# Performance work log

Measured on AMD Instinct MI355X. Metric: run time of the kernel, lower is better.

Reference implementation:

```python
import jax, jax.numpy as jnp
import numpy as np

HIDDEN = 1024
HEADS = 16
HEAD_DIM = HIDDEN // HEADS  # 64
BATCH = 2
SEQ = 2048
MASK_IDENTITY = True


def setup_inputs() -> dict:
    key = jax.random.key(0)
    ks = jax.random.split(key, 9)
    s = 1.0 / np.sqrt(HIDDEN)
    return {
        "hidden_states": jax.random.normal(ks[0], (BATCH, SEQ, HIDDEN), jnp.float32),
        "Wq": jax.random.normal(ks[1], (HIDDEN, HIDDEN), jnp.float32) * s,
        "bq": jnp.zeros((HIDDEN,), jnp.float32),
        "Wk": jax.random.normal(ks[2], (HIDDEN, HIDDEN), jnp.float32) * s,
        "bk": jnp.zeros((HIDDEN,), jnp.float32),
        "Wv": jax.random.normal(ks[3], (HIDDEN, HIDDEN), jnp.float32) * s,
        "bv": jnp.zeros((HIDDEN,), jnp.float32),
        "Wd": jax.random.normal(ks[4], (HIDDEN, HIDDEN), jnp.float32) * s,
        "bd": jnp.zeros((HIDDEN,), jnp.float32),
    }


def _split_heads(x):
    # [B, S, H*Dh] -> [B, H, S, Dh]
    b, s, _ = x.shape
    return x.reshape(b, s, HEADS, HEAD_DIM).transpose(0, 2, 1, 3)


def reference(hidden_states, Wq, bq, Wk, bk, Wv, bv, Wd, bd):
    # torch Linear: y = x @ W.T + b
    q = _split_heads(hidden_states @ Wq.T + bq)  # [B,H,S,Dh]
    k = _split_heads(hidden_states @ Wk.T + bk)
    v = _split_heads(hidden_states @ Wv.T + bv)

    scores = jnp.einsum("bhqd,bhkd->bhqk", q, k) / np.sqrt(HEAD_DIM)
    if MASK_IDENTITY:
        mask_value = -jnp.finfo(scores.dtype).max
        eye = jnp.eye(scores.shape[-1], dtype=bool)  # [S,S], broadcast over B,H
        scores = jnp.where(eye, mask_value, scores)
    probs = jax.nn.softmax(scores, axis=-1)
    ctx = jnp.einsum("bhqk,bhkd->bhqd", probs, v)  # [B,H,S,Dh]
    b, h, s, d = ctx.shape
    ctx = ctx.transpose(0, 2, 1, 3).reshape(b, s, h * d)  # [B,S,H*Dh]
    return ctx @ Wd.T + bd
```

## Files before the change

kernel.cpp:

```cpp
#include <hip/hip_runtime.h>
#include <hip/hip_bf16.h>
#include <stdint.h>

#define HIDDEN 1024
#define SEQL   2048
#define NB     2
#define NH     16
#define DH     64
#define MTOT   (NB * SEQL)
#define QKVLD  3072
#define SCALE_Q 0.18033688011112042f

typedef __bf16 bf16x8 __attribute__((ext_vector_type(8)));
typedef __bf16 bf16x4 __attribute__((ext_vector_type(4)));
typedef float  f32x4  __attribute__((ext_vector_type(4)));
typedef float  f32x16 __attribute__((ext_vector_type(16)));

__device__ __forceinline__ void gload16(const void* g, void* l) {
    __builtin_amdgcn_global_load_lds(
        (const __attribute__((address_space(1))) void*)g,
        (__attribute__((address_space(3))) void*)l, 16, 0, 0);
}
__device__ __forceinline__ float exp2fast(float x) {
    float r;
    asm("v_exp_f32 %0, %1" : "=v"(r) : "v"(x));
    return r;
}
__device__ __forceinline__ unsigned cvtpk(float lo, float hi) {
    unsigned r;
    asm("v_cvt_pk_bf16_f32 %0, %1, %2" : "=v"(r) : "v"(lo), "v"(hi));
    return r;
}
__device__ __forceinline__ void pswap(unsigned& a, unsigned& b) {
    asm volatile("v_permlane32_swap_b32 %0, %1" : "+v"(a), "+v"(b));
}

__global__ void prep(const float* __restrict__ H,
                     const float* __restrict__ Wq, const float* __restrict__ Wk,
                     const float* __restrict__ Wv, const float* __restrict__ Wd,
                     const float* __restrict__ bq, const float* __restrict__ bk,
                     const float* __restrict__ bv,
                     __bf16* __restrict__ Hb, __bf16* __restrict__ Wall,
                     float* __restrict__ bqkv) {
    const int bid = blockIdx.x, tid = threadIdx.x;
    if (bid < 4096) {
        int i = bid * 256 + tid;
        float4 v = reinterpret_cast<const float4*>(H)[i];
        bf16x4 o = { (__bf16)v.x, (__bf16)v.y, (__bf16)v.z, (__bf16)v.w };
        reinterpret_cast<bf16x4*>(Hb)[i] = o;
    } else if (bid < 8192) {
        int wi = bid - 4096;
        int seg = wi >> 10;
        int i = (wi & 1023) * 256 + tid;
        const float* src = seg == 0 ? Wq : seg == 1 ? Wk : seg == 2 ? Wv : Wd;
        float sc = (seg == 0) ? SCALE_Q : 1.0f;
        float4 v = reinterpret_cast<const float4*>(src)[i];
        bf16x4 o = { (__bf16)(v.x * sc), (__bf16)(v.y * sc),
                     (__bf16)(v.z * sc), (__bf16)(v.w * sc) };
        reinterpret_cast<bf16x4*>(Wall)[(size_t)seg * 262144 + i] = o;
    } else {
        for (int i = tid; i < 3072; i += 256) {
            float v = (i < 1024) ? bq[i] * SCALE_Q
                    : (i < 2048) ? bk[i - 1024] : bv[i - 2048];
            bqkv[i] = v;
        }
    }
}

__global__ __launch_bounds__(256) void transpose_v(const __bf16* __restrict__ QKV,
                                                   __bf16* __restrict__ Vt) {
    __shared__ __bf16 t[64][66];
    const int st = blockIdx.x, bh = blockIdx.y;
    const int b = bh >> 4, h = bh & 15;
    const int tid = threadIdx.x;
    const int r = tid >> 3, c = tid & 7;
    const __bf16* src = QKV + (size_t)(b * SEQL + st * 64) * QKVLD + 2048 + h * 64;
    *(int4*)&t[r][c * 8]      = *(const int4*)(src + (size_t)r * QKVLD + c * 8);
    *(int4*)&t[r + 32][c * 8] = *(const int4*)(src + (size_t)(r + 32) * QKVLD + c * 8);
    __syncthreads();
    __bf16* dst = Vt + (size_t)bh * DH * SEQL + st * 64;
    const int d = tid >> 3;
    __bf16 tmp0[8], tmp1[8];
#pragma unroll
    for (int j = 0; j < 8; ++j) {
        tmp0[j] = t[c * 8 + j][d];
        tmp1[j] = t[c * 8 + j][d + 32];
    }
    *(int4*)(dst + (size_t)d * SEQL + c * 8)        = *(int4*)tmp0;
    *(int4*)(dst + (size_t)(d + 32) * SEQL + c * 8) = *(int4*)tmp1;
}

__global__ __launch_bounds__(256) void gemm_qkv(const __bf16* __restrict__ A,
                                                const __bf16* __restrict__ Bw,
                                                const float* __restrict__ bias,
                                                __bf16* __restrict__ C) {
    __shared__ __bf16 As[128 * 32];
    __shared__ __bf16 Bs[128 * 32];
    const int K = 1024, N = QKVLD;

    int bid = blockIdx.x;
    int swz = (bid & 7) * 96 + (bid >> 3);
    const int bm = (swz & 31) * 128;
    const int bn = (swz >> 5) * 128;

    const int tid = threadIdx.x;
    const int w = tid >> 6, l = tid & 63, g = l >> 4, lc = l & 15;
    const int wr = (w >> 1) * 64, wc = (w & 1) * 64;
    const int row = tid >> 2, ch = tid & 3;

    const __bf16* Ap = A  + (size_t)(bm + row) * K + ch * 8;
    const __bf16* Bp = Bw + (size_t)(bn + row) * K + ch * 8;
    __bf16* AsLo = &As[w * 512];
    __bf16* AsHi = &As[2048 + w * 512];
    __bf16* BsLo = &Bs[w * 512];
    __bf16* BsHi = &Bs[2048 + w * 512];

    f32x4 acc[4][4];
    const f32x4 z4 = {0.f, 0.f, 0.f, 0.f};
#pragma unroll
    for (int i = 0; i < 4; ++i)
#pragma unroll
        for (int j = 0; j < 4; ++j) acc[i][j] = z4;

    for (int kt = 0; kt < K; kt += 32) {
        gload16(Ap + kt,                   AsLo);
        gload16(Ap + kt + (size_t)64 * K,  AsHi);
        gload16(Bp + kt,                   BsLo);
        gload16(Bp + kt + (size_t)64 * K,  BsHi);
        __syncthreads();

        bf16x8 af[4], bfr[4];
#pragma unroll
        for (int i = 0; i < 4; ++i)
            af[i] = *(const bf16x8*)&As[(wr + i * 16 + lc) * 32 + g * 8];
#pragma unroll
        for (int j = 0; j < 4; ++j)
            bfr[j] = *(const bf16x8*)&Bs[(wc + j * 16 + lc) * 32 + g * 8];
        __builtin_amdgcn_s_setprio(1);
#pragma unroll
        for (int i = 0; i < 4; ++i)
#pragma unroll
            for (int j = 0; j < 4; ++j)
                acc[i][j] = __builtin_amdgcn_mfma_f32_16x16x32_bf16(af[i], bfr[j], acc[i][j], 0, 0, 0);
        __builtin_amdgcn_s_setprio(0);
        __syncthreads();
    }

#pragma unroll
    for (int i = 0; i < 4; ++i) {
        int r0 = bm + wr + i * 16 + g * 4;
#pragma unroll
        for (int j = 0; j < 4; ++j) {
            int c = bn + wc + j * 16 + lc;
            float bb = bias[c];
#pragma unroll
            for (int r = 0; r < 4; ++r)
                C[(size_t)(r0 + r) * N + c] = (__bf16)(acc[i][j][r] + bb);
        }
    }
}

__global__ __launch_bounds__(256) void gemm_out(const __bf16* __restrict__ A,
                                                const __bf16* __restrict__ Bw,
                                                const float* __restrict__ bias,
                                                float* __restrict__ Cout) {
    __shared__ __bf16 As[64 * 32];
    __shared__ __bf16 Bs[128 * 32];
    const int K = 1024, N = 1024;

    int bid = blockIdx.x;
    int swz = (bid & 7) * 64 + (bid >> 3);
    const int bm = (swz & 63) * 64;
    const int bn = (swz >> 6) * 128;

    const int tid = threadIdx.x;
    const int w = tid >> 6, l = tid & 63, g = l >> 4, lc = l & 15;
    const int wr = (w >> 1) * 32, wc = (w & 1) * 64;
    const int row = tid >> 2, ch = tid & 3;

    const __bf16* Ap = A  + (size_t)(bm + row) * K + ch * 8;
    const __bf16* Bp = Bw + (size_t)(bn + row) * K + ch * 8;
    __bf16* AsW  = &As[w * 512];
    __bf16* BsLo = &Bs[w * 512];
    __bf16* BsHi = &Bs[2048 + w * 512];

    f32x4 acc[2][4];
    const f32x4 z4 = {0.f, 0.f, 0.f, 0.f};
#pragma unroll
    for (int i = 0; i < 2; ++i)
#pragma unroll
        for (int j = 0; j < 4; ++j) acc[i][j] = z4;

    for (int kt = 0; kt < K; kt += 32) {
        gload16(Ap + kt,                   AsW);
        gload16(Bp + kt,                   BsLo);
        gload16(Bp + kt + (size_t)64 * K,  BsHi);
        __syncthreads();

        bf16x8 af[2], bfr[4];
#pragma unroll
        for (int i = 0; i < 2; ++i)
            af[i] = *(const bf16x8*)&As[(wr + i * 16 + lc) * 32 + g * 8];
#pragma unroll
        for (int j = 0; j < 4; ++j)
            bfr[j] = *(const bf16x8*)&Bs[(wc + j * 16 + lc) * 32 + g * 8];
        __builtin_amdgcn_s_setprio(1);
#pragma unroll
        for (int i = 0; i < 2; ++i)
#pragma unroll
            for (int j = 0; j < 4; ++j)
                acc[i][j] = __builtin_amdgcn_mfma_f32_16x16x32_bf16(af[i], bfr[j], acc[i][j], 0, 0, 0);
        __builtin_amdgcn_s_setprio(0);
        __syncthreads();
    }

#pragma unroll
    for (int i = 0; i < 2; ++i) {
        int r0 = bm + wr + i * 16 + g * 4;
#pragma unroll
        for (int j = 0; j < 4; ++j) {
            int c = bn + wc + j * 16 + lc;
            float bb = bias[c];
#pragma unroll
            for (int r = 0; r < 4; ++r)
                Cout[(size_t)(r0 + r) * N + c] = acc[i][j][r] + bb;
        }
    }
}

__global__ __launch_bounds__(256) void attn_kernel(const __bf16* __restrict__ QKV,
                                                   const __bf16* __restrict__ Vt,
                                                   __bf16* __restrict__ Ctx) {
    __shared__ __bf16 k_lds[2][64][64];
    __shared__ __bf16 v_lds[2][64][64];
    __shared__ float  bc[4][32];

    const int tid = threadIdx.x;
    const int w  = tid >> 6;
    const int l  = tid & 63;
    const int ql = l & 31;
    const int lh = l >> 5;

    int bid = blockIdx.x;
    int swz = (bid & 7) * 64 + (bid >> 3);
    const int qt = swz & 15, bh = swz >> 4;
    const int b = bh >> 4, hd = bh & 15;
    const int qw = qt * 128 + w * 32;

    const __bf16* Qg = QKV + (size_t)b * SEQL * QKVLD + hd * DH;
    const __bf16* Kg = Qg + 1024;
    const __bf16* Vg = Vt + (size_t)bh * DH * SEQL;

    bf16x8 qf[4];
    {
        const __bf16* qp = Qg + (size_t)(qw + ql) * QKVLD + lh * 8;
#pragma unroll
        for (int c = 0; c < 4; ++c) qf[c] = *(const bf16x8*)(qp + c * 16);
    }

    const int sr   = l >> 3;
    const int gcol = ((l & 7) * 8) ^ (sr << 3);
    auto stage = [&](int kb, int nb) {
        const __bf16* kp = Kg + (size_t)(kb + w * 8 + sr) * QKVLD + gcol;
        const __bf16* vp = Vg + (size_t)(w * 8 + sr) * SEQL + kb + gcol;
        gload16(kp,                          &k_lds[nb][w * 8][0]);
        gload16(kp + (size_t)32 * QKVLD,     &k_lds[nb][32 + w * 8][0]);
        gload16(vp,                          &v_lds[nb][w * 8][0]);
        gload16(vp + (size_t)32 * SEQL,      &v_lds[nb][32 + w * 8][0]);
    };

    stage(0, 0);
    __syncthreads();

    f32x16 o0, o1;
#pragma unroll
    for (int r = 0; r < 16; ++r) { o0[r] = 0.f; o1[r] = 0.f; }
    float l8[8];
#pragma unroll
    for (int r = 0; r < 8; ++r) l8[r] = 0.f;

    f32x16 zc;
#pragma unroll
    for (int r = 0; r < 16; ++r) zc[r] = 0.f;

    const int NT = SEQL / 64;
    const int rsw = (ql & 7) << 3;

    for (int kt = 0; kt < NT; ++kt) {
        const int buf = kt & 1;
        const int kb = kt * 64;

        if (kt + 1 < NT) stage(kb + 64, buf ^ 1);

        f32x16 sA, sB;
        __builtin_amdgcn_s_setprio(1);
        {
            bf16x8 k0 = *(const bf16x8*)&k_lds[buf][ql]     [(lh * 8) ^ rsw];
            bf16x8 k1 = *(const bf16x8*)&k_lds[buf][32 + ql][(lh * 8) ^ rsw];
            sA = __builtin_amdgcn_mfma_f32_32x32x16_bf16(k0, qf[0], zc, 0, 0, 0);
            sB = __builtin_amdgcn_mfma_f32_32x32x16_bf16(k1, qf[0], zc, 0, 0, 0);
        }
#pragma unroll
        for (int c = 1; c < 4; ++c) {
            bf16x8 k0 = *(const bf16x8*)&k_lds[buf][ql]     [(c * 16 + lh * 8) ^ rsw];
            bf16x8 k1 = *(const bf16x8*)&k_lds[buf][32 + ql][(c * 16 + lh * 8) ^ rsw];
            sA = __builtin_amdgcn_mfma_f32_32x32x16_bf16(k0, qf[c], sA, 0, 0, 0);
            sB = __builtin_amdgcn_mfma_f32_32x32x16_bf16(k1, qf[c], sB, 0, 0, 0);
        }
        __builtin_amdgcn_s_setprio(0);

        if (kb < qw + 32 && qw < kb + 64) {
            const int qg = qw + ql;
#pragma unroll
            for (int i = 0; i < 16; ++i) {
                int kg = kb + (i & 3) + ((i >> 2) & 3) * 8 + lh * 4;
                if (kg == qg)      sA[i] = -1e30f;
                if (kg + 32 == qg) sB[i] = -1e30f;
            }
        }

#pragma unroll
        for (int i = 0; i < 16; ++i) sA[i] = exp2fast(sA[i]);
#pragma unroll
        for (int i = 0; i < 16; ++i) sB[i] = exp2fast(sB[i]);
#pragma unroll
        for (int i = 0; i < 8; ++i)
            l8[i] += (sA[i] + sA[i + 8]) + (sB[i] + sB[i + 8]);

        bf16x8 pa[4];
        {
            unsigned w0 = cvtpk(sA[0],  sA[1]);
            unsigned w1 = cvtpk(sA[2],  sA[3]);
            unsigned w2 = cvtpk(sA[4],  sA[5]);
            unsigned w3 = cvtpk(sA[6],  sA[7]);
            unsigned w4 = cvtpk(sA[8],  sA[9]);
            unsigned w5 = cvtpk(sA[10], sA[11]);
            unsigned w6 = cvtpk(sA[12], sA[13]);
            unsigned w7 = cvtpk(sA[14], sA[15]);
            pswap(w0, w2); pswap(w1, w3);
            pswap(w4, w6); pswap(w5, w7);
            uint4 lo4 = {w0, w1, w2, w3};
            uint4 hi4 = {w4, w5, w6, w7};
            pa[0] = *(bf16x8*)&lo4;
            pa[1] = *(bf16x8*)&hi4;
        }
        {
            unsigned w0 = cvtpk(sB[0],  sB[1]);
            unsigned w1 = cvtpk(sB[2],  sB[3]);
            unsigned w2 = cvtpk(sB[4],  sB[5]);
            unsigned w3 = cvtpk(sB[6],  sB[7]);
            unsigned w4 = cvtpk(sB[8],  sB[9]);
            unsigned w5 = cvtpk(sB[10], sB[11]);
            unsigned w6 = cvtpk(sB[12], sB[13]);
            unsigned w7 = cvtpk(sB[14], sB[15]);
            pswap(w0, w2); pswap(w1, w3);
            pswap(w4, w6); pswap(w5, w7);
            uint4 lo4 = {w0, w1, w2, w3};
            uint4 hi4 = {w4, w5, w6, w7};
            pa[2] = *(bf16x8*)&lo4;
            pa[3] = *(bf16x8*)&hi4;
        }

        __builtin_amdgcn_s_setprio(1);
#pragma unroll
        for (int s = 0; s < 2; ++s)
#pragma unroll
            for (int sl = 0; sl < 2; ++sl) {
                const int col = s * 32 + sl * 16 + lh * 8;
                bf16x8 v0 = *(const bf16x8*)&v_lds[buf][ql]     [col ^ rsw];
                bf16x8 v1 = *(const bf16x8*)&v_lds[buf][32 + ql][col ^ rsw];
                o0 = __builtin_amdgcn_mfma_f32_32x32x16_bf16(pa[s * 2 + sl], v0, o0, 0, 0, 0);
                o1 = __builtin_amdgcn_mfma_f32_32x32x16_bf16(pa[s * 2 + sl], v1, o1, 0, 0, 0);
            }
        __builtin_amdgcn_s_setprio(0);

        __syncthreads();
    }

    float l_r = ((l8[0] + l8[1]) + (l8[2] + l8[3]))
              + ((l8[4] + l8[5]) + (l8[6] + l8[7]));
    l_r += __shfl_xor(l_r, 32, 64);
    if (lh == 0) bc[w][ql] = 1.f / l_r;
    asm volatile("s_waitcnt lgkmcnt(0)" ::: "memory");
    __builtin_amdgcn_wave_barrier();
#pragma unroll
    for (int r = 0; r < 16; ++r) {
        int cr = (r & 3) + (r >> 2) * 8 + lh * 4;
        float iv = bc[w][cr];
        int qrow = qw + cr;
        __bf16* cp = Ctx + (size_t)(b * SEQL + qrow) * HIDDEN + hd * DH + ql;
        cp[0]  = (__bf16)(o0[r] * iv);
        cp[32] = (__bf16)(o1[r] * iv);
    }
}

extern "C" void kernel_launch(void* const* d_in, const int* in_sizes, int n_in,
                              void* d_out, int out_size, void* d_ws, size_t ws_size,
                              hipStream_t stream) {
    const float* H  = (const float*)d_in[0];
    const float* Wq = (const float*)d_in[1];
    const float* bq = (const float*)d_in[2];
    const float* Wk = (const float*)d_in[3];
    const float* bk = (const float*)d_in[4];
    const float* Wv = (const float*)d_in[5];
    const float* bv = (const float*)d_in[6];
    const float* Wd = (const float*)d_in[7];
    const float* bd = (const float*)d_in[8];
    float* out = (float*)d_out;

    char* ws = (char*)d_ws;
    const size_t MB = 1024 * 1024;
    __bf16* Hb    = (__bf16*)(ws + 0 * MB);
    __bf16* Ctx   = (__bf16*)(ws + 0 * MB);
    __bf16* Wqkvb = (__bf16*)(ws + 8 * MB);
    __bf16* Wdb   = (__bf16*)(ws + 14 * MB);
    float*  bqkv  = (float*) (ws + 16 * MB);
    __bf16* QKV   = (__bf16*)(ws + 17 * MB);
    __bf16* Vtb   = (__bf16*)(ws + 41 * MB);
    if (ws_size < 49 * MB) return;

    prep<<<8193, 256, 0, stream>>>(H, Wq, Wk, Wv, Wd, bq, bk, bv, Hb, Wqkvb, bqkv);

    gemm_qkv<<<768, 256, 0, stream>>>(Hb, Wqkvb, bqkv, QKV);

    transpose_v<<<dim3(32, 32), 256, 0, stream>>>(QKV, Vtb);

    attn_kernel<<<512, 256, 0, stream>>>(QKV, Vtb, Ctx);

    gemm_out<<<512, 256, 0, stream>>>(Ctx, Wdb, bd, out);
}
```

Before: 131.3 us.

## Double K-tile depth in QKV GEMM and attention key block size with swizzled LDS

The QKV projection GEMM now stages 64-wide K slices instead of 32, with an XOR-swizzled LDS layout, so it runs half as many barrier pairs per output tile. The attention kernel now stages 128 keys per iteration instead of 64 and processes them as two 64-key sub-blocks, with a new swizzle for the wider V tile. Both changes aim to cut synchronisation and loop overhead per unit of work. In exchange they double LDS use per block, which may lower occupancy.

```diff
diff --git a/kernel.cpp b/kernel.cpp
--- a/kernel.cpp
+++ b/kernel.cpp
@@ -94,8 +94,8 @@
                                                 const __bf16* __restrict__ Bw,
                                                 const float* __restrict__ bias,
                                                 __bf16* __restrict__ C) {
-    __shared__ __bf16 As[128 * 32];
-    __shared__ __bf16 Bs[128 * 32];
+    __shared__ __bf16 As[128 * 64];
+    __shared__ __bf16 Bs[128 * 64];
     const int K = 1024, N = QKVLD;
 
     int bid = blockIdx.x;
@@ -106,14 +106,13 @@
     const int tid = threadIdx.x;
     const int w = tid >> 6, l = tid & 63, g = l >> 4, lc = l & 15;
     const int wr = (w >> 1) * 64, wc = (w & 1) * 64;
-    const int row = tid >> 2, ch = tid & 3;
-
-    const __bf16* Ap = A  + (size_t)(bm + row) * K + ch * 8;
-    const __bf16* Bp = Bw + (size_t)(bn + row) * K + ch * 8;
-    __bf16* AsLo = &As[w * 512];
-    __bf16* AsHi = &As[2048 + w * 512];
-    __bf16* BsLo = &Bs[w * 512];
-    __bf16* BsHi = &Bs[2048 + w * 512];
+
+    const int sr = l >> 3;
+    const int scol = ((l & 7) ^ sr) * 8;
+    const __bf16* Ap = A  + (size_t)(bm + w * 8 + sr) * K + scol;
+    const __bf16* Bp = Bw + (size_t)(bn + w * 8 + sr) * K + scol;
+
+    const int rswa = (lc & 7) * 8;
 
     f32x4 acc[4][4];
     const f32x4 z4 = {0.f, 0.f, 0.f, 0.f};
@@ -122,26 +121,33 @@
 #pragma unroll
         for (int j = 0; j < 4; ++j) acc[i][j] = z4;
 
-    for (int kt = 0; kt < K; kt += 32) {
-        gload16(Ap + kt,                   AsLo);
-        gload16(Ap + kt + (size_t)64 * K,  AsHi);
-        gload16(Bp + kt,                   BsLo);
-        gload16(Bp + kt + (size_t)64 * K,  BsHi);
+    for (int kt = 0; kt < K; kt += 64) {
+#pragma unroll
+        for (int q = 0; q < 4; ++q) {
+            gload16(Ap + kt + (size_t)(32 * q) * K, &As[(w * 8 + 32 * q) * 64]);
+            gload16(Bp + kt + (size_t)(32 * q) * K, &Bs[(w * 8 + 32 * q) * 64]);
+        }
         __syncthreads();
 
-        bf16x8 af[4], bfr[4];
-#pragma unroll
-        for (int i = 0; i < 4; ++i)
-            af[i] = *(const bf16x8*)&As[(wr + i * 16 + lc) * 32 + g * 8];
-#pragma unroll
-        for (int j = 0; j < 4; ++j)
-            bfr[j] = *(const bf16x8*)&Bs[(wc + j * 16 + lc) * 32 + g * 8];
+        bf16x8 af[4][2], bfr[4][2];
+#pragma unroll
+        for (int i = 0; i < 4; ++i) {
+            const int ra = (wr + i * 16 + lc) * 64;
+            const int rb = (wc + i * 16 + lc) * 64;
+#pragma unroll
+            for (int kk = 0; kk < 2; ++kk) {
+                af[i][kk]  = *(const bf16x8*)&As[ra + ((kk * 32 + g * 8) ^ rswa)];
+                bfr[i][kk] = *(const bf16x8*)&Bs[rb + ((kk * 32 + g * 8) ^ rswa)];
+            }
+        }
         __builtin_amdgcn_s_setprio(1);
 #pragma unroll
-        for (int i = 0; i < 4; ++i)
-#pragma unroll
-            for (int j = 0; j < 4; ++j)
-                acc[i][j] = __builtin_amdgcn_mfma_f32_16x16x32_bf16(af[i], bfr[j], acc[i][j], 0, 0, 0);
+        for (int kk = 0; kk < 2; ++kk)
+#pragma unroll
+            for (int i = 0; i < 4; ++i)
+#pragma unroll
+                for (int j = 0; j < 4; ++j)
+                    acc[i][j] = __builtin_amdgcn_mfma_f32_16x16x32_bf16(af[i][kk], bfr[j][kk], acc[i][j], 0, 0, 0);
         __builtin_amdgcn_s_setprio(0);
         __syncthreads();
     }
@@ -231,8 +237,8 @@
 __global__ __launch_bounds__(256) void attn_kernel(const __bf16* __restrict__ QKV,
                                                    const __bf16* __restrict__ Vt,
                                                    __bf16* __restrict__ Ctx) {
-    __shared__ __bf16 k_lds[2][64][64];
-    __shared__ __bf16 v_lds[2][64][64];
+    __shared__ __bf16 k_lds[2][128][64];
+    __shared__ __bf16 v_lds[2][64][128];
     __shared__ float  bc[4][32];
 
     const int tid = threadIdx.x;
@@ -259,14 +265,23 @@
     }
 
     const int sr   = l >> 3;
-    const int gcol = ((l & 7) * 8) ^ (sr << 3);
+    const int gcol = ((l & 7) ^ sr) * 8;
+    const int vr  = l >> 4;
+    const int vch = l & 15;
+
     auto stage = [&](int kb, int nb) {
-        const __bf16* kp = Kg + (size_t)(kb + w * 8 + sr) * QKVLD + gcol;
-        const __bf16* vp = Vg + (size_t)(w * 8 + sr) * SEQL + kb + gcol;
-        gload16(kp,                          &k_lds[nb][w * 8][0]);
-        gload16(kp + (size_t)32 * QKVLD,     &k_lds[nb][32 + w * 8][0]);
-        gload16(vp,                          &v_lds[nb][w * 8][0]);
-        gload16(vp + (size_t)32 * SEQL,      &v_lds[nb][32 + w * 8][0]);
+#pragma unroll
+        for (int q = 0; q < 4; ++q) {
+            gload16(Kg + (size_t)(kb + w * 8 + 32 * q + sr) * QKVLD + gcol,
+                    &k_lds[nb][w * 8 + 32 * q][0]);
+        }
+#pragma unroll
+        for (int q = 0; q < 4; ++q) {
+            int drow = w * 16 + 4 * q + vr;
+            int vchunk = vch ^ (drow & 7);
+            gload16(Vg + (size_t)drow * SEQL + kb + vchunk * 8,
+                    &v_lds[nb][w * 16 + 4 * q][0]);
+        }
     };
 
     stage(0, 0);
@@ -283,96 +298,102 @@
 #pragma unroll
     for (int r = 0; r < 16; ++r) zc[r] = 0.f;
 
-    const int NT = SEQL / 64;
+    const int NT = SEQL / 128;
     const int rsw = (ql & 7) << 3;
 
     for (int kt = 0; kt < NT; ++kt) {
         const int buf = kt & 1;
-        const int kb = kt * 64;
-
-        if (kt + 1 < NT) stage(kb + 64, buf ^ 1);
-
-        f32x16 sA, sB;
-        __builtin_amdgcn_s_setprio(1);
-        {
-            bf16x8 k0 = *(const bf16x8*)&k_lds[buf][ql]     [(lh * 8) ^ rsw];
-            bf16x8 k1 = *(const bf16x8*)&k_lds[buf][32 + ql][(lh * 8) ^ rsw];
-            sA = __builtin_amdgcn_mfma_f32_32x32x16_bf16(k0, qf[0], zc, 0, 0, 0);
-            sB = __builtin_amdgcn_mfma_f32_32x32x16_bf16(k1, qf[0], zc, 0, 0, 0);
-        }
-#pragma unroll
-        for (int c = 1; c < 4; ++c) {
-            bf16x8 k0 = *(const bf16x8*)&k_lds[buf][ql]     [(c * 16 + lh * 8) ^ rsw];
-            bf16x8 k1 = *(const bf16x8*)&k_lds[buf][32 + ql][(c * 16 + lh * 8) ^ rsw];
-            sA = __builtin_amdgcn_mfma_f32_32x32x16_bf16(k0, qf[c], sA, 0, 0, 0);
-            sB = __builtin_amdgcn_mfma_f32_32x32x16_bf16(k1, qf[c], sB, 0, 0, 0);
-        }
-        __builtin_amdgcn_s_setprio(0);
-
-        if (kb < qw + 32 && qw < kb + 64) {
-            const int qg = qw + ql;
-#pragma unroll
-            for (int i = 0; i < 16; ++i) {
-                int kg = kb + (i & 3) + ((i >> 2) & 3) * 8 + lh * 4;
-                if (kg == qg)      sA[i] = -1e30f;
-                if (kg + 32 == qg) sB[i] = -1e30f;
-            }
-        }
-
-#pragma unroll
-        for (int i = 0; i < 16; ++i) sA[i] = exp2fast(sA[i]);
-#pragma unroll
-        for (int i = 0; i < 16; ++i) sB[i] = exp2fast(sB[i]);
-#pragma unroll
-        for (int i = 0; i < 8; ++i)
-            l8[i] += (sA[i] + sA[i + 8]) + (sB[i] + sB[i + 8]);
-
-        bf16x8 pa[4];
-        {
-            unsigned w0 = cvtpk(sA[0],  sA[1]);
-            unsigned w1 = cvtpk(sA[2],  sA[3]);
-            unsigned w2 = cvtpk(sA[4],  sA[5]);
-            unsigned w3 = cvtpk(sA[6],  sA[7]);
-            unsigned w4 = cvtpk(sA[8],  sA[9]);
-            unsigned w5 = cvtpk(sA[10], sA[11]);
-            unsigned w6 = cvtpk(sA[12], sA[13]);
-            unsigned w7 = cvtpk(sA[14], sA[15]);
-            pswap(w0, w2); pswap(w1, w3);
-            pswap(w4, w6); pswap(w5, w7);
-            uint4 lo4 = {w0, w1, w2, w3};
-            uint4 hi4 = {w4, w5, w6, w7};
-            pa[0] = *(bf16x8*)&lo4;
-            pa[1] = *(bf16x8*)&hi4;
-        }
-        {
-            unsigned w0 = cvtpk(sB[0],  sB[1]);
-            unsigned w1 = cvtpk(sB[2],  sB[3]);
-            unsigned w2 = cvtpk(sB[4],  sB[5]);
-            unsigned w3 = cvtpk(sB[6],  sB[7]);
-            unsigned w4 = cvtpk(sB[8],  sB[9]);
-            unsigned w5 = cvtpk(sB[10], sB[11]);
-            unsigned w6 = cvtpk(sB[12], sB[13]);
-            unsigned w7 = cvtpk(sB[14], sB[15]);
-            pswap(w0, w2); pswap(w1, w3);
-            pswap(w4, w6); pswap(w5, w7);
-            uint4 lo4 = {w0, w1, w2, w3};
-            uint4 hi4 = {w4, w5, w6, w7};
-            pa[2] = *(bf16x8*)&lo4;
-            pa[3] = *(bf16x8*)&hi4;
-        }
-
-        __builtin_amdgcn_s_setprio(1);
-#pragma unroll
-        for (int s = 0; s < 2; ++s)
-#pragma unroll
-            for (int sl = 0; sl < 2; ++sl) {
-                const int col = s * 32 + sl * 16 + lh * 8;
-                bf16x8 v0 = *(const bf16x8*)&v_lds[buf][ql]     [col ^ rsw];
-                bf16x8 v1 = *(const bf16x8*)&v_lds[buf][32 + ql][col ^ rsw];
-                o0 = __builtin_amdgcn_mfma_f32_32x32x16_bf16(pa[s * 2 + sl], v0, o0, 0, 0, 0);
-                o1 = __builtin_amdgcn_mfma_f32_32x32x16_bf16(pa[s * 2 + sl], v1, o1, 0, 0, 0);
-            }
-        __builtin_amdgcn_s_setprio(0);
+        const int kb = kt * 128;
+
+        if (kt + 1 < NT) stage(kb + 128, buf ^ 1);
+
+#pragma unroll
+        for (int sub = 0; sub < 2; ++sub) {
+            const int kbs = kb + sub * 64;
+            const int ro  = sub * 64;
+
+            f32x16 sA, sB;
+            __builtin_amdgcn_s_setprio(1);
+            {
+                bf16x8 k0 = *(const bf16x8*)&k_lds[buf][ro + ql]     [(lh * 8) ^ rsw];
+                bf16x8 k1 = *(const bf16x8*)&k_lds[buf][ro + 32 + ql][(lh * 8) ^ rsw];
+                sA = __builtin_amdgcn_mfma_f32_32x32x16_bf16(k0, qf[0], zc, 0, 0, 0);
+                sB = __builtin_amdgcn_mfma_f32_32x32x16_bf16(k1, qf[0], zc, 0, 0, 0);
+            }
+#pragma unroll
+            for (int c = 1; c < 4; ++c) {
+                bf16x8 k0 = *(const bf16x8*)&k_lds[buf][ro + ql]     [(c * 16 + lh * 8) ^ rsw];
+                bf16x8 k1 = *(const bf16x8*)&k_lds[buf][ro + 32 + ql][(c * 16 + lh * 8) ^ rsw];
+                sA = __builtin_amdgcn_mfma_f32_32x32x16_bf16(k0, qf[c], sA, 0, 0, 0);
+                sB = __builtin_amdgcn_mfma_f32_32x32x16_bf16(k1, qf[c], sB, 0, 0, 0);
+            }
+            __builtin_amdgcn_s_setprio(0);
+
+            if (kbs < qw + 32 && qw < kbs + 64) {
+                const int qg = qw + ql;
+#pragma unroll
+                for (int i = 0; i < 16; ++i) {
+                    int kg = kbs + (i & 3) + ((i >> 2) & 3) * 8 + lh * 4;
+                    if (kg == qg)      sA[i] = -1e30f;
+                    if (kg + 32 == qg) sB[i] = -1e30f;
+                }
+            }
+
+#pragma unroll
+            for (int i = 0; i < 16; ++i) sA[i] = exp2fast(sA[i]);
+#pragma unroll
+            for (int i = 0; i < 16; ++i) sB[i] = exp2fast(sB[i]);
+#pragma unroll
+            for (int i = 0; i < 8; ++i)
+                l8[i] += (sA[i] + sA[i + 8]) + (sB[i] + sB[i + 8]);
+
+            bf16x8 pa[4];
+            {
+                unsigned w0 = cvtpk(sA[0],  sA[1]);
+                unsigned w1 = cvtpk(sA[2],  sA[3]);
+                unsigned w2 = cvtpk(sA[4],  sA[5]);
+                unsigned w3 = cvtpk(sA[6],  sA[7]);
+                unsigned w4 = cvtpk(sA[8],  sA[9]);
+                unsigned w5 = cvtpk(sA[10], sA[11]);
+                unsigned w6 = cvtpk(sA[12], sA[13]);
+                unsigned w7 = cvtpk(sA[14], sA[15]);
+                pswap(w0, w2); pswap(w1, w3);
+                pswap(w4, w6); pswap(w5, w7);
+                uint4 lo4 = {w0, w1, w2, w3};
+                uint4 hi4 = {w4, w5, w6, w7};
+                pa[0] = *(bf16x8*)&lo4;
+                pa[1] = *(bf16x8*)&hi4;
+            }
+            {
+                unsigned w0 = cvtpk(sB[0],  sB[1]);
+                unsigned w1 = cvtpk(sB[2],  sB[3]);
+                unsigned w2 = cvtpk(sB[4],  sB[5]);
+                unsigned w3 = cvtpk(sB[6],  sB[7]);
+                unsigned w4 = cvtpk(sB[8],  sB[9]);
+                unsigned w5 = cvtpk(sB[10], sB[11]);
+                unsigned w6 = cvtpk(sB[12], sB[13]);
+                unsigned w7 = cvtpk(sB[14], sB[15]);
+                pswap(w0, w2); pswap(w1, w3);
+                pswap(w4, w6); pswap(w5, w7);
+                uint4 lo4 = {w0, w1, w2, w3};
+                uint4 hi4 = {w4, w5, w6, w7};
+                pa[2] = *(bf16x8*)&lo4;
+                pa[3] = *(bf16x8*)&hi4;
+            }
+
+            __builtin_amdgcn_s_setprio(1);
+#pragma unroll
+            for (int s = 0; s < 2; ++s)
+#pragma unroll
+                for (int sl = 0; sl < 2; ++sl) {
+                    const int col = sub * 64 + s * 32 + sl * 16 + lh * 8;
+                    bf16x8 v0 = *(const bf16x8*)&v_lds[buf][ql]     [col ^ rsw];
+                    bf16x8 v1 = *(const bf16x8*)&v_lds[buf][32 + ql][col ^ rsw];
+                    o0 = __builtin_amdgcn_mfma_f32_32x32x16_bf16(pa[s * 2 + sl], v0, o0, 0, 0, 0);
+                    o1 = __builtin_amdgcn_mfma_f32_32x32x16_bf16(pa[s * 2 + sl], v1, o1, 0, 0, 0);
+                }
+            __builtin_amdgcn_s_setprio(0);
+        }
 
         __syncthreads();
     }
```

After: 128.6 us. 2.0% less time.

## Enlarge attention blocks to 8 waves and 128-key tiles per barrier

Applied to the files above, without the earlier changes.

The attention kernel now runs 512-thread blocks covering 256 query rows, and each iteration stages a 128-key K/V tile processed as two 64-key sub-steps. This halves the number of block barriers and gives twice as many waves to share each staged K/V tile, cutting redundant global loads. The V LDS layout and swizzle are reworked for 128-wide rows. The trade-off is double the LDS per block, only 256 blocks on the device, and coarser barriers that could reduce latency hiding.

```diff
diff --git a/kernel.cpp b/kernel.cpp
--- a/kernel.cpp
+++ b/kernel.cpp
@@ -228,12 +228,12 @@
     }
 }
 
-__global__ __launch_bounds__(256) void attn_kernel(const __bf16* __restrict__ QKV,
+__global__ __launch_bounds__(512) void attn_kernel(const __bf16* __restrict__ QKV,
                                                    const __bf16* __restrict__ Vt,
                                                    __bf16* __restrict__ Ctx) {
-    __shared__ __bf16 k_lds[2][64][64];
-    __shared__ __bf16 v_lds[2][64][64];
-    __shared__ float  bc[4][32];
+    __shared__ __bf16 k_lds[2][128][64];
+    __shared__ __bf16 v_lds[2][64][128];
+    __shared__ float  bc[8][32];
 
     const int tid = threadIdx.x;
     const int w  = tid >> 6;
@@ -242,10 +242,10 @@
     const int lh = l >> 5;
 
     int bid = blockIdx.x;
-    int swz = (bid & 7) * 64 + (bid >> 3);
-    const int qt = swz & 15, bh = swz >> 4;
+    int swz = (bid & 7) * 32 + (bid >> 3);
+    const int qt = swz & 7, bh = swz >> 3;
     const int b = bh >> 4, hd = bh & 15;
-    const int qw = qt * 128 + w * 32;
+    const int qw = qt * 256 + w * 32;
 
     const __bf16* Qg = QKV + (size_t)b * SEQL * QKVLD + hd * DH;
     const __bf16* Kg = Qg + 1024;
@@ -259,14 +259,16 @@
     }
 
     const int sr   = l >> 3;
-    const int gcol = ((l & 7) * 8) ^ (sr << 3);
+    const int gcol = ((l & 7) ^ sr) * 8;
+    const int vr  = l >> 4;
+    const int vch = l & 15;
     auto stage = [&](int kb, int nb) {
-        const __bf16* kp = Kg + (size_t)(kb + w * 8 + sr) * QKVLD + gcol;
-        const __bf16* vp = Vg + (size_t)(w * 8 + sr) * SEQL + kb + gcol;
-        gload16(kp,                          &k_lds[nb][w * 8][0]);
-        gload16(kp + (size_t)32 * QKVLD,     &k_lds[nb][32 + w * 8][0]);
-        gload16(vp,                          &v_lds[nb][w * 8][0]);
-        gload16(vp + (size_t)32 * SEQL,      &v_lds[nb][32 + w * 8][0]);
+        gload16(Kg + (size_t)(kb + w * 8 + sr) * QKVLD + gcol,      &k_lds[nb][w * 8][0]);
+        gload16(Kg + (size_t)(kb + 64 + w * 8 + sr) * QKVLD + gcol, &k_lds[nb][64 + w * 8][0]);
+        int dr0 = w * 4 + vr;
+        int dr1 = 32 + w * 4 + vr;
+        gload16(Vg + (size_t)dr0 * SEQL + kb + (vch ^ (dr0 & 7)) * 8, &v_lds[nb][w * 4][0]);
+        gload16(Vg + (size_t)dr1 * SEQL + kb + (vch ^ (dr1 & 7)) * 8, &v_lds[nb][32 + w * 4][0]);
     };
 
     stage(0, 0);
@@ -283,96 +285,102 @@
 #pragma unroll
     for (int r = 0; r < 16; ++r) zc[r] = 0.f;
 
-    const int NT = SEQL / 64;
+    const int NT = SEQL / 128;
     const int rsw = (ql & 7) << 3;
 
     for (int kt = 0; kt < NT; ++kt) {
         const int buf = kt & 1;
-        const int kb = kt * 64;
-
-        if (kt + 1 < NT) stage(kb + 64, buf ^ 1);
-
-        f32x16 sA, sB;
-        __builtin_amdgcn_s_setprio(1);
-        {
-            bf16x8 k0 = *(const bf16x8*)&k_lds[buf][ql]     [(lh * 8) ^ rsw];
-            bf16x8 k1 = *(const bf16x8*)&k_lds[buf][32 + ql][(lh * 8) ^ rsw];
-            sA = __builtin_amdgcn_mfma_f32_32x32x16_bf16(k0, qf[0], zc, 0, 0, 0);
-            sB = __builtin_amdgcn_mfma_f32_32x32x16_bf16(k1, qf[0], zc, 0, 0, 0);
+        const int kb = kt * 128;
+
+        if (kt + 1 < NT) stage(kb + 128, buf ^ 1);
+
+#pragma unroll
+        for (int sub = 0; sub < 2; ++sub) {
+            const int kbs = kb + sub * 64;
+            const int ro  = sub * 64;
+
+            f32x16 sA, sB;
+            __builtin_amdgcn_s_setprio(1);
+            {
+                bf16x8 k0 = *(const bf16x8*)&k_lds[buf][ro + ql]     [(lh * 8) ^ rsw];
+                bf16x8 k1 = *(const bf16x8*)&k_lds[buf][ro + 32 + ql][(lh * 8) ^ rsw];
+                sA = __builtin_amdgcn_mfma_f32_32x32x16_bf16(k0, qf[0], zc, 0, 0, 0);
+                sB = __builtin_amdgcn_mfma_f32_32x32x16_bf16(k1, qf[0], zc, 0, 0, 0);
+            }
+#pragma unroll
+            for (int c = 1; c < 4; ++c) {
+                bf16x8 k0 = *(const bf16x8*)&k_lds[buf][ro + ql]     [(c * 16 + lh * 8) ^ rsw];
+                bf16x8 k1 = *(const bf16x8*)&k_lds[buf][ro + 32 + ql][(c * 16 + lh * 8) ^ rsw];
+                sA = __builtin_amdgcn_mfma_f32_32x32x16_bf16(k0, qf[c], sA, 0, 0, 0);
+                sB = __builtin_amdgcn_mfma_f32_32x32x16_bf16(k1, qf[c], sB, 0, 0, 0);
+            }
+            __builtin_amdgcn_s_setprio(0);
+
+            if (kbs < qw + 32 && qw < kbs + 64) {
+                const int qg = qw + ql;
+#pragma unroll
+                for (int i = 0; i < 16; ++i) {
+                    int kg = kbs + (i & 3) + ((i >> 2) & 3) * 8 + lh * 4;
+                    if (kg == qg)      sA[i] = -1e30f;
+                    if (kg + 32 == qg) sB[i] = -1e30f;
+                }
+            }
+
+#pragma unroll
+            for (int i = 0; i < 16; ++i) sA[i] = exp2fast(sA[i]);
+#pragma unroll
+            for (int i = 0; i < 16; ++i) sB[i] = exp2fast(sB[i]);
+#pragma unroll
+            for (int i = 0; i < 8; ++i)
+                l8[i] += (sA[i] + sA[i + 8]) + (sB[i] + sB[i + 8]);
+
+            bf16x8 pa[4];
+            {
+                unsigned w0 = cvtpk(sA[0],  sA[1]);
+                unsigned w1 = cvtpk(sA[2],  sA[3]);
+                unsigned w2 = cvtpk(sA[4],  sA[5]);
+                unsigned w3 = cvtpk(sA[6],  sA[7]);
+                unsigned w4 = cvtpk(sA[8],  sA[9]);
+                unsigned w5 = cvtpk(sA[10], sA[11]);
+                unsigned w6 = cvtpk(sA[12], sA[13]);
+                unsigned w7 = cvtpk(sA[14], sA[15]);
+                pswap(w0, w2); pswap(w1, w3);
+                pswap(w4, w6); pswap(w5, w7);
+                uint4 lo4 = {w0, w1, w2, w3};
+                uint4 hi4 = {w4, w5, w6, w7};
+                pa[0] = *(bf16x8*)&lo4;
+                pa[1] = *(bf16x8*)&hi4;
+            }
+            {
+                unsigned w0 = cvtpk(sB[0],  sB[1]);
+                unsigned w1 = cvtpk(sB[2],  sB[3]);
+                unsigned w2 = cvtpk(sB[4],  sB[5]);
+                unsigned w3 = cvtpk(sB[6],  sB[7]);
+                unsigned w4 = cvtpk(sB[8],  sB[9]);
+                unsigned w5 = cvtpk(sB[10], sB[11]);
+                unsigned w6 = cvtpk(sB[12], sB[13]);
+                unsigned w7 = cvtpk(sB[14], sB[15]);
+                pswap(w0, w2); pswap(w1, w3);
+                pswap(w4, w6); pswap(w5, w7);
+                uint4 lo4 = {w0, w1, w2, w3};
+                uint4 hi4 = {w4, w5, w6, w7};
+                pa[2] = *(bf16x8*)&lo4;
+                pa[3] = *(bf16x8*)&hi4;
+            }
+
+            __builtin_amdgcn_s_setprio(1);
+#pragma unroll
+            for (int s = 0; s < 2; ++s)
+#pragma unroll
+                for (int sl = 0; sl < 2; ++sl) {
+                    const int col = sub * 64 + s * 32 + sl * 16 + lh * 8;
+                    bf16x8 v0 = *(const bf16x8*)&v_lds[buf][ql]     [col ^ rsw];
+                    bf16x8 v1 = *(const bf16x8*)&v_lds[buf][32 + ql][col ^ rsw];
+                    o0 = __builtin_amdgcn_mfma_f32_32x32x16_bf16(pa[s * 2 + sl], v0, o0, 0, 0, 0);
+                    o1 = __builtin_amdgcn_mfma_f32_32x32x16_bf16(pa[s * 2 + sl], v1, o1, 0, 0, 0);
+                }
+            __builtin_amdgcn_s_setprio(0);
         }
-#pragma unroll
-        for (int c = 1; c < 4; ++c) {
-            bf16x8 k0 = *(const bf16x8*)&k_lds[buf][ql]     [(c * 16 + lh * 8) ^ rsw];
-            bf16x8 k1 = *(const bf16x8*)&k_lds[buf][32 + ql][(c * 16 + lh * 8) ^ rsw];
-            sA = __builtin_amdgcn_mfma_f32_32x32x16_bf16(k0, qf[c], sA, 0, 0, 0);
-            sB = __builtin_amdgcn_mfma_f32_32x32x16_bf16(k1, qf[c], sB, 0, 0, 0);
-        }
-        __builtin_amdgcn_s_setprio(0);
-
-        if (kb < qw + 32 && qw < kb + 64) {
-            const int qg = qw + ql;
-#pragma unroll
-            for (int i = 0; i < 16; ++i) {
-                int kg = kb + (i & 3) + ((i >> 2) & 3) * 8 + lh * 4;
-                if (kg == qg)      sA[i] = -1e30f;
-                if (kg + 32 == qg) sB[i] = -1e30f;
-            }
-        }
-
-#pragma unroll
-        for (int i = 0; i < 16; ++i) sA[i] = exp2fast(sA[i]);
-#pragma unroll
-        for (int i = 0; i < 16; ++i) sB[i] = exp2fast(sB[i]);
-#pragma unroll
-        for (int i = 0; i < 8; ++i)
-            l8[i] += (sA[i] + sA[i + 8]) + (sB[i] + sB[i + 8]);
-
-        bf16x8 pa[4];
-        {
-            unsigned w0 = cvtpk(sA[0],  sA[1]);
-            unsigned w1 = cvtpk(sA[2],  sA[3]);
-            unsigned w2 = cvtpk(sA[4],  sA[5]);
-            unsigned w3 = cvtpk(sA[6],  sA[7]);
-            unsigned w4 = cvtpk(sA[8],  sA[9]);
-            unsigned w5 = cvtpk(sA[10], sA[11]);
-            unsigned w6 = cvtpk(sA[12], sA[13]);
-            unsigned w7 = cvtpk(sA[14], sA[15]);
-            pswap(w0, w2); pswap(w1, w3);
-            pswap(w4, w6); pswap(w5, w7);
-            uint4 lo4 = {w0, w1, w2, w3};
-            uint4 hi4 = {w4, w5, w6, w7};
-            pa[0] = *(bf16x8*)&lo4;
-            pa[1] = *(bf16x8*)&hi4;
-        }
-        {
-            unsigned w0 = cvtpk(sB[0],  sB[1]);
-            unsigned w1 = cvtpk(sB[2],  sB[3]);
-            unsigned w2 = cvtpk(sB[4],  sB[5]);
-            unsigned w3 = cvtpk(sB[6],  sB[7]);
-            unsigned w4 = cvtpk(sB[8],  sB[9]);
-            unsigned w5 = cvtpk(sB[10], sB[11]);
-            unsigned w6 = cvtpk(sB[12], sB[13]);
-            unsigned w7 = cvtpk(sB[14], sB[15]);
-            pswap(w0, w2); pswap(w1, w3);
-            pswap(w4, w6); pswap(w5, w7);
-            uint4 lo4 = {w0, w1, w2, w3};
-            uint4 hi4 = {w4, w5, w6, w7};
-            pa[2] = *(bf16x8*)&lo4;
-            pa[3] = *(bf16x8*)&hi4;
-        }
-
-        __builtin_amdgcn_s_setprio(1);
-#pragma unroll
-        for (int s = 0; s < 2; ++s)
-#pragma unroll
-            for (int sl = 0; sl < 2; ++sl) {
-                const int col = s * 32 + sl * 16 + lh * 8;
-                bf16x8 v0 = *(const bf16x8*)&v_lds[buf][ql]     [col ^ rsw];
-                bf16x8 v1 = *(const bf16x8*)&v_lds[buf][32 + ql][col ^ rsw];
-                o0 = __builtin_amdgcn_mfma_f32_32x32x16_bf16(pa[s * 2 + sl], v0, o0, 0, 0, 0);
-                o1 = __builtin_amdgcn_mfma_f32_32x32x16_bf16(pa[s * 2 + sl], v1, o1, 0, 0, 0);
-            }
-        __builtin_amdgcn_s_setprio(0);
 
         __syncthreads();
     }
@@ -425,7 +433,7 @@
 
     transpose_v<<<dim3(32, 32), 256, 0, stream>>>(QKV, Vtb);
 
-    attn_kernel<<<512, 256, 0, stream>>>(QKV, Vtb, Ctx);
+    attn_kernel<<<256, 512, 0, stream>>>(QKV, Vtb, Ctx);
 
     gemm_out<<<512, 256, 0, stream>>>(Ctx, Wdb, bd, out);
 }
```

New measurement: 119.9 us. -8.6%, faster.
